# Performance work log

Hardware: AMD Instinct MI355X
Metric: run time of the kernel (lower is better)

Reference implementation:

```python
import jax, jax.numpy as jnp
import numpy as np

B, C, H, W = 4, 128, 256, 256
N, NPOS, KS = 4000, 8, 3
CH = 2 * NPOS  # mask=False -> 2*n_pos offset channels


def setup_inputs() -> dict:
    key = jax.random.key(0)
    ks = jax.random.split(key, 8)
    x = jax.random.normal(ks[0], (B, C, H, W), jnp.float32)
    keypoints = jax.random.uniform(ks[1], (B, N, 2), jnp.float32) * 2.0 - 1.0  # [-1,1]
    w1 = jax.random.normal(ks[2], (CH, C, KS, KS), jnp.float32) * 0.05  # offset conv 3x3
    b1 = jnp.zeros((CH,), jnp.float32)
    w2 = jax.random.normal(ks[3], (CH, CH), jnp.float32) * 0.05        # offset conv 1x1
    b2 = jnp.zeros((CH,), jnp.float32)
    wsf = jax.random.normal(ks[4], (C, C), jnp.float32) * 0.05         # sf_conv 1x1 no bias
    agg_weights = jax.random.uniform(ks[5], (NPOS, C, C), jnp.float32)  # torch.rand init
    return {"x": x, "keypoints": keypoints, "w1": w1, "b1": b1, "w2": w2,
            "b2": b2, "wsf": wsf, "agg_weights": agg_weights}


def _bilinear_sample(img, px, py):
    """grid_sample(mode=bilinear, align_corners=True, padding=zeros) at pixel coords.
    img: (C,H,W); px,py: (M,). Returns (C,M)."""
    c, h, w = img.shape
    x0f = jnp.floor(px); y0f = jnp.floor(py)
    x0 = x0f.astype(jnp.int32); y0 = y0f.astype(jnp.int32)
    wx1 = px - x0f; wx0 = 1.0 - wx1
    wy1 = py - y0f; wy0 = 1.0 - wy1

    def tap(xi, yi, wgt):
        valid = ((xi >= 0) & (xi < w) & (yi >= 0) & (yi < h)).astype(img.dtype)
        v = img[:, jnp.clip(yi, 0, h - 1), jnp.clip(xi, 0, w - 1)]  # (C,M)
        return v * (wgt * valid)

    return (tap(x0, y0, wx0 * wy0) + tap(x0 + 1, y0, wx1 * wy0)
            + tap(x0, y0 + 1, wx0 * wy1) + tap(x0 + 1, y0 + 1, wx1 * wy1))


def _per_image(xi, kpts, w1, b1, w2, b2, wsf, agg_weights):
    wh = jnp.array([W - 1.0, H - 1.0], xi.dtype)
    max_offset = max(H, W) / 4.0
    kwh = (kpts / 2.0 + 0.5) * wh                      # (N,2) pixel coords, >=0
    rc = kwh.astype(jnp.int32)                          # .long() trunc (positive)
    corner = jnp.trunc(rc.astype(jnp.float32) - KS / 2.0 + 1.0).astype(jnp.int32)
    cx = jnp.clip(corner[:, 0], 0, W - 1 - KS)
    cy = jnp.clip(corner[:, 1], 0, H - 1 - KS)
    ar = jnp.arange(KS)
    # patch[n,c,a,b] = xi[c, cy_n+a, cx_n+b]
    patch = xi[:, (cy[:, None] + ar)[:, :, None], (cx[:, None] + ar)[:, None, :]]  # (C,N,KS,KS)
    patch = patch.transpose(1, 0, 2, 3)                 # (N,C,KS,KS)
    # offset network: 3x3 conv (valid) on 3x3 patch == full contraction, then ReLU, 1x1 conv
    h1 = jax.nn.relu(jnp.einsum('nchw,ochw->no', patch, w1) + b1)
    off = jnp.clip(h1 @ w2.T + b2, -max_offset, max_offset)  # (N, 2*NPOS)
    off = off.reshape(-1, 2, NPOS).transpose(0, 2, 1)        # (N,NPOS,2)
    # deform sampling positions; torch normalizes then grid_sample(align_corners=True)
    # maps exactly back to pixel coords, so sample at pixel coords directly
    pos = kwh[:, None, :] + off                              # (N,NPOS,2)
    feats = _bilinear_sample(xi, pos[..., 0].reshape(-1), pos[..., 1].reshape(-1))  # (C,N*NPOS)
    feats = feats.reshape(C, -1, NPOS).transpose(1, 0, 2)    # (N,C,NPOS)
    feats = jax.nn.selu(jnp.einsum('ncp,dc->ndp', feats, wsf))
    descs = jnp.einsum('ncp,pcd->nd', feats, agg_weights)    # (N,C)
    descs = descs / jnp.maximum(jnp.linalg.norm(descs, axis=1, keepdims=True), 1e-12)
    return descs, off


def reference(x, keypoints, w1, b1, w2, b2, wsf, agg_weights):
    f = jax.vmap(lambda xi, k: _per_image(xi, k, w1, b1, w2, b2, wsf, agg_weights))
    descriptors, offsets = f(x, keypoints)
    return descriptors, offsets  # (B,N,C), (B,N,NPOS,2)
```

## Files before the change

kernel.cpp:

```cpp
#include <hip/hip_runtime.h>
#include <math.h>

#define BB 4
#define CC 128
#define HH 256
#define WW 256
#define NN 4000
#define NPOS 8
#define KS 3
#define HWSZ (HH*WW)

#define SELU_ALPHA 1.6732632423543772f
#define SELU_SCALE 1.0507009873554805f
#define MAX_OFFSET 64.0f

typedef unsigned short ushort_t;
typedef short short8 __attribute__((ext_vector_type(8)));
typedef float f32x4 __attribute__((ext_vector_type(4)));
typedef unsigned short ushort4_t __attribute__((ext_vector_type(4)));
typedef unsigned short ushort8_t __attribute__((ext_vector_type(8)));

#define XT_ELEMS    ((size_t)BB*HH*WW*CC)
#define WSFBF_ELEMS ((size_t)CC*CC)
#define AGGT_ELEMS  ((size_t)NPOS*CC*CC)
#define W1T_ELEMS   ((size_t)16*CC*9)
#define WS_NEEDED   ((XT_ELEMS+WSFBF_ELEMS+AGGT_ELEMS+W1T_ELEMS)*sizeof(ushort_t))

__device__ __forceinline__ ushort_t f2bf(float f) {
    unsigned u = __builtin_bit_cast(unsigned, f);
    unsigned r = (u + 0x7FFFu + ((u >> 16) & 1u)) >> 16;
    return (ushort_t)r;
}
__device__ __forceinline__ float bf2f(ushort_t u) {
    return __builtin_bit_cast(float, ((unsigned)u) << 16);
}

__global__ __launch_bounds__(256) void k0p(
    const float* __restrict__ x, ushort_t* __restrict__ xt,
    const float* __restrict__ wsf, const float* __restrict__ agg,
    const float* __restrict__ w1,
    ushort_t* __restrict__ wsf_bf, ushort_t* __restrict__ aggT_bf,
    ushort_t* __restrict__ w1t_bf)
{
    int blk = blockIdx.x;
    const int t = threadIdx.x;
    if (blk >= BB * HH * 4) {
        int i = (blk - BB * HH * 4) * 256 + t;
        if (i < CC * CC) wsf_bf[i] = f2bf(wsf[i]);
        if (i < NPOS * CC * CC) {
            int p = i >> 14, d = (i >> 7) & 127, c = i & 127;
            aggT_bf[i] = f2bf(agg[(p << 14) + (c << 7) + d]);
        }
        if (i < 16 * 1152) {
            int o = i / 1152, e = i - o * 1152, k = e >> 7, c = e & 127;
            w1t_bf[i] = f2bf(w1[o * 1152 + c * 9 + k]);
        }
        return;
    }
    int xc = blk & 3, y = (blk >> 2) & 255, b = blk >> 10;
    int x0 = xc * 64;
    __shared__ ushort_t lds[64][136];

    const float* xb = x + (size_t)b * CC * HWSZ + (size_t)y * WW + x0;
    for (int v = t; v < 2048; v += 256) {
        int c = v >> 4, xo4 = v & 15;
        float4 val = *(const float4*)(xb + (size_t)c * HWSZ + xo4 * 4);
        lds[xo4*4+0][c] = f2bf(val.x);
        lds[xo4*4+1][c] = f2bf(val.y);
        lds[xo4*4+2][c] = f2bf(val.z);
        lds[xo4*4+3][c] = f2bf(val.w);
    }
    __syncthreads();
    ushort_t* outb = xt + ((size_t)b * HWSZ + (size_t)y * WW + x0) * CC;
    for (int v = t; v < 2048; v += 256) {
        int xo = v >> 5, c4 = v & 31;
        ushort4_t val;
        val[0] = lds[xo][c4*4+0];
        val[1] = lds[xo][c4*4+1];
        val[2] = lds[xo][c4*4+2];
        val[3] = lds[xo][c4*4+3];
        *(ushort4_t*)(outb + (size_t)xo * CC + c4 * 4) = val;
    }
}

__global__ __launch_bounds__(256, 2) void k14_fused(
    const ushort_t* __restrict__ xt, const float* __restrict__ kpts,
    const ushort_t* __restrict__ w1t_bf, const float* __restrict__ b1,
    const float* __restrict__ w2, const float* __restrict__ b2,
    const ushort_t* __restrict__ wsf_bf, const ushort_t* __restrict__ aggT_bf,
    float* __restrict__ out_desc, float* __restrict__ out_off)
{
    const int t    = threadIdx.x;
    const int wv   = t >> 6;
    const int lane = t & 63;
    const int m    = lane & 15;
    const int q    = lane >> 4;
    const int n0   = blockIdx.x * 16;
    const int b    = n0 / NN;
    const ushort_t* xb = xt + (size_t)b * HWSZ * CC;

    __shared__ ushort_t fg[CC * CC];
    union PT {
        float partials[4][16][16];
        struct { int tapoff[128][4]; float tapw[128][4]; } tp;
    };
    __shared__ PT    upt;
    __shared__ float h1f[16][17];
    __shared__ float offs[16][16];
    __shared__ float kw[16][2];
    __shared__ int   cxy[16][2];
    __shared__ float wsum[4][16];
    __shared__ float rn[16];

    if (t < 16) {
        float kx = kpts[(size_t)(n0 + t) * 2 + 0];
        float ky = kpts[(size_t)(n0 + t) * 2 + 1];
        float kwx = (kx * 0.5f + 0.5f) * (float)(WW - 1);
        float kwy = (ky * 0.5f + 0.5f) * (float)(HH - 1);
        kw[t][0] = kwx; kw[t][1] = kwy;
        int rcx = (int)kwx, rcy = (int)kwy;
        int cx = (int)truncf((float)rcx - 0.5f);
        int cy = (int)truncf((float)rcy - 0.5f);
        cxy[t][0] = min(max(cx, 0), WW - 1 - KS);
        cxy[t][1] = min(max(cy, 0), HH - 1 - KS);
    }
    __syncthreads();

    {
        int px0 = cxy[m][0], py0 = cxy[m][1];
        const ushort_t* brow = w1t_bf + m * 1152 + wv * 288 + q * 8;
        short8 a0, a1, a2, a3, a4, a5, a6, a7, a8;
        #define LOAD_A(idx, dst) { \
            int e = wv * 288 + (idx) * 32 + q * 8; \
            int k = e >> 7, c = e & 127; \
            int kd = k / 3, kx2 = k - kd * 3; \
            dst = *(const short8*)(xb + ((size_t)((py0 + kd) * WW + px0 + kx2)) * CC + c); }
        LOAD_A(0, a0) LOAD_A(1, a1) LOAD_A(2, a2) LOAD_A(3, a3) LOAD_A(4, a4)
        LOAD_A(5, a5) LOAD_A(6, a6) LOAD_A(7, a7) LOAD_A(8, a8)
        #undef LOAD_A
        f32x4 hacc = {0.f, 0.f, 0.f, 0.f};
        #define MF(idx, areg) { \
            short8 bfr = *(const short8*)(brow + (idx) * 32); \
            hacc = __builtin_amdgcn_mfma_f32_16x16x32_bf16(areg, bfr, hacc, 0, 0, 0); }
        MF(0, a0) MF(1, a1) MF(2, a2) MF(3, a3) MF(4, a4)
        MF(5, a5) MF(6, a6) MF(7, a7) MF(8, a8)
        #undef MF
        #pragma unroll
        for (int r = 0; r < 4; ++r) upt.partials[wv][q * 4 + r][m] = hacc[r];
    }
    __syncthreads();
    {
        int kp = t >> 4, o = t & 15;
        float h = upt.partials[0][kp][o] + upt.partials[1][kp][o]
                + upt.partials[2][kp][o] + upt.partials[3][kp][o] + b1[o];
        h1f[kp][o] = fmaxf(h, 0.f);
    }
    __syncthreads();
    {
        int kp = t >> 4, j = t & 15;
        float s = b2[j];
        #pragma unroll
        for (int o = 0; o < 16; ++o) s += h1f[kp][o] * w2[j * 16 + o];
        s = fminf(fmaxf(s, -MAX_OFFSET), MAX_OFFSET);
        offs[kp][j] = s;
        int p = j & 7, comp = j >> 3;
        out_off[((size_t)(n0 + kp) * 8 + p) * 2 + comp] = s;
    }
    __syncthreads();

    if (t < 128) {
        int kp = t >> 3, p = t & 7;
        float px = kw[kp][0] + offs[kp][p];
        float py = kw[kp][1] + offs[kp][8 + p];
        float x0f = floorf(px), y0f = floorf(py);
        int x0 = (int)x0f, y0 = (int)y0f;
        float wx1 = px - x0f, wx0 = 1.f - wx1;
        float wy1 = py - y0f, wy0 = 1.f - wy1;
        int x0c = min(max(x0, 0), WW - 1);
        int x1c = min(max(x0 + 1, 0), WW - 1);
        int y0c = min(max(y0, 0), HH - 1);
        int y1c = min(max(y0 + 1, 0), HH - 1);
        float vx0 = (x0 >= 0 && x0 < WW) ? 1.f : 0.f;
        float vx1 = (x0 + 1 >= 0 && x0 + 1 < WW) ? 1.f : 0.f;
        float vy0 = (y0 >= 0 && y0 < HH) ? 1.f : 0.f;
        float vy1 = (y0 + 1 >= 0 && y0 + 1 < HH) ? 1.f : 0.f;
        upt.tp.tapoff[t][0] = (y0c * WW + x0c) * CC;
        upt.tp.tapoff[t][1] = (y0c * WW + x1c) * CC;
        upt.tp.tapoff[t][2] = (y1c * WW + x0c) * CC;
        upt.tp.tapoff[t][3] = (y1c * WW + x1c) * CC;
        upt.tp.tapw[t][0] = wx0 * wy0 * vx0 * vy0;
        upt.tp.tapw[t][1] = wx1 * wy0 * vx1 * vy0;
        upt.tp.tapw[t][2] = wx0 * wy1 * vx0 * vy1;
        upt.tp.tapw[t][3] = wx1 * wy1 * vx1 * vy1;
    }
    __syncthreads();

    {
        const int grp = t >> 4;
        const int cl  = t & 15;
        #pragma unroll
        for (int half = 0; half < 2; ++half) {
            ushort8_t tv0[4], tv1[4], tv2[4], tv3[4];
            float4 twv[4];
            #pragma unroll
            for (int i = 0; i < 4; ++i) {
                int pair = (half * 4 + i) * 16 + grp;
                const int* to = upt.tp.tapoff[pair];
                twv[i] = *(const float4*)upt.tp.tapw[pair];
                tv0[i] = *(const ushort8_t*)(xb + to[0] + cl * 8);
                tv1[i] = *(const ushort8_t*)(xb + to[1] + cl * 8);
                tv2[i] = *(const ushort8_t*)(xb + to[2] + cl * 8);
                tv3[i] = *(const ushort8_t*)(xb + to[3] + cl * 8);
            }
            #pragma unroll
            for (int i = 0; i < 4; ++i) {
                int pair = (half * 4 + i) * 16 + grp;
                float w00 = twv[i].x, w01 = twv[i].y, w10 = twv[i].z, w11 = twv[i].w;
                ushort8_t out;
                #pragma unroll
                for (int j = 0; j < 8; ++j) {
                    float v = bf2f(tv0[i][j]) * w00;
                    v += bf2f(tv1[i][j]) * w01;
                    v += bf2f(tv2[i][j]) * w10;
                    v += bf2f(tv3[i][j]) * w11;
                    out[j] = f2bf(v);
                }
                unsigned byte = ((unsigned)(pair * 256 + cl * 16))
                              ^ (((unsigned)(pair & 7)) << 4);
                *(ushort8_t*)((char*)fg + byte) = out;
            }
        }
    }
    __syncthreads();

    for (int rti = 0; rti < 2; ++rti) {
        int rt = wv * 2 + rti;
        int r  = rt * 16 + m;
        unsigned key = ((unsigned)(r & 7)) << 4;
        short8 afr[4];
        #pragma unroll
        for (int kk = 0; kk < 4; ++kk) {
            unsigned byte = ((unsigned)(r * 256 + q * 16 + kk * 64)) ^ key;
            afr[kk] = *(const short8*)((const char*)fg + byte);
        }
        for (int ct = 0; ct < 8; ++ct) {
            const ushort_t* brow = wsf_bf + (ct * 16 + m) * CC + q * 8;
            f32x4 acc = {0.f, 0.f, 0.f, 0.f};
            #pragma unroll
            for (int kk = 0; kk < 4; ++kk) {
                short8 bfr = *(const short8*)(brow + kk * 32);
                acc = __builtin_amdgcn_mfma_f32_16x16x32_bf16(afr[kk], bfr, acc, 0, 0, 0);
            }
            #pragma unroll
            for (int rr = 0; rr < 4; ++rr) {
                float s = acc[rr];
                s = (s > 0.f) ? (SELU_SCALE * s)
                              : (SELU_SCALE * SELU_ALPHA * (expf(s) - 1.f));
                int row = rt * 16 + q * 4 + rr;
                int col = ct * 16 + m;
                unsigned byte = ((unsigned)(row * 256 + col * 2))
                              ^ (((unsigned)((row >> 3) & 7)) << 4);
                *(ushort_t*)((char*)fg + byte) = f2bf(s);
            }
        }
    }
    __syncthreads();

    f32x4 acc2[2];
    acc2[0] = (f32x4){0.f, 0.f, 0.f, 0.f};
    acc2[1] = (f32x4){0.f, 0.f, 0.f, 0.f};
    const int ctbase = wv * 2;
    for (int kk = 0; kk < 32; ++kk) {
        int p    = kk >> 2;
        int rowA = m * 8 + p;
        unsigned byte = ((unsigned)(rowA * 256 + (kk & 3) * 64 + q * 16))
                      ^ (((unsigned)((rowA >> 3) & 7)) << 4);
        short8 afr = *(const short8*)((const char*)fg + byte);
        #pragma unroll
        for (int i = 0; i < 2; ++i) {
            int ct = ctbase + i;
            const ushort_t* brow = aggT_bf + (size_t)(p * CC + ct * 16 + m) * CC
                                 + (kk & 3) * 32 + q * 8;
            short8 bfr = *(const short8*)brow;
            acc2[i] = __builtin_amdgcn_mfma_f32_16x16x32_bf16(afr, bfr, acc2[i], 0, 0, 0);
        }
    }

    {
        float ss[4];
        #pragma unroll
        for (int rr = 0; rr < 4; ++rr)
            ss[rr] = acc2[0][rr] * acc2[0][rr] + acc2[1][rr] * acc2[1][rr];
        #pragma unroll
        for (int mask = 1; mask <= 8; mask <<= 1) {
            #pragma unroll
            for (int rr = 0; rr < 4; ++rr) ss[rr] += __shfl_xor(ss[rr], mask);
        }
        if (m == 0) {
            #pragma unroll
            for (int rr = 0; rr < 4; ++rr) wsum[wv][q * 4 + rr] = ss[rr];
        }
    }
    __syncthreads();
    if (t < 16) {
        float tot = wsum[0][t] + wsum[1][t] + wsum[2][t] + wsum[3][t];
        rn[t] = 1.0f / fmaxf(sqrtf(tot), 1e-12f);
    }
    __syncthreads();
    {
        #pragma unroll
        for (int i = 0; i < 2; ++i) {
            int col = (ctbase + i) * 16 + m;
            #pragma unroll
            for (int rr = 0; rr < 4; ++rr) {
                int n = q * 4 + rr;
                out_desc[(size_t)(n0 + n) * CC + col] = acc2[i][rr] * rn[n];
            }
        }
    }
}

__global__ __launch_bounds__(256, 4) void sddh_baseline(
    const float* __restrict__ x, const float* __restrict__ keypoints,
    const float* __restrict__ w1, const float* __restrict__ b1,
    const float* __restrict__ w2, const float* __restrict__ b2,
    const float* __restrict__ wsf, const float* __restrict__ agg,
    float* __restrict__ out_desc, float* __restrict__ out_off)
{
    const int bn = blockIdx.x;
    const int b  = bn / NN;
    const int t  = threadIdx.x;
    const float* xi = x + (size_t)b * CC * HWSZ;

    __shared__ float patch[CC * 9];
    __shared__ float conv_part[16][17];
    __shared__ float h1s[16];
    __shared__ float offs[16];
    __shared__ float feats[CC][NPOS];
    __shared__ float cpart2[CC][NPOS];
    __shared__ float g[CC][NPOS];
    __shared__ float dpart[CC];
    __shared__ float desc[CC];
    __shared__ float sq[128];
    __shared__ float kxy[2];

    if (t == 0) {
        float kx = keypoints[(size_t)bn * 2 + 0];
        float ky = keypoints[(size_t)bn * 2 + 1];
        kxy[0] = (kx * 0.5f + 0.5f) * (float)(WW - 1);
        kxy[1] = (ky * 0.5f + 0.5f) * (float)(HH - 1);
    }
    __syncthreads();
    const float kwx = kxy[0], kwy = kxy[1];
    const int rcx = (int)kwx, rcy = (int)kwy;
    int cx = (int)truncf((float)rcx - 0.5f);
    int cy = (int)truncf((float)rcy - 0.5f);
    cx = min(max(cx, 0), WW - 1 - KS);
    cy = min(max(cy, 0), HH - 1 - KS);

    for (int e = t; e < CC * 9; e += 256) {
        int c = e / 9, k = e % 9;
        int dy = k / 3, dx = k % 3;
        patch[e] = xi[(size_t)c * HWSZ + (cy + dy) * WW + (cx + dx)];
    }
    __syncthreads();
    {
        int o = t & 15, j = t >> 4;
        float acc = 0.f;
        const float* wo = w1 + o * (CC * 9);
        for (int e = j; e < CC * 9; e += 16) acc += patch[e] * wo[e];
        conv_part[o][j] = acc;
    }
    __syncthreads();
    if (t < 16) {
        float s = b1[t];
        #pragma unroll
        for (int j = 0; j < 16; j++) s += conv_part[t][j];
        h1s[t] = fmaxf(s, 0.f);
    }
    __syncthreads();
    if (t < 16) {
        float s = b2[t];
        #pragma unroll
        for (int k = 0; k < 16; k++) s += h1s[k] * w2[t * 16 + k];
        s = fminf(fmaxf(s, -MAX_OFFSET), MAX_OFFSET);
        offs[t] = s;
        int idx = (t < 8) ? (bn * 16 + t * 2) : (bn * 16 + (t - 8) * 2 + 1);
        out_off[idx] = s;
    }
    __syncthreads();

    for (int e = t; e < CC * NPOS; e += 256) {
        int c = e & 127, p = e >> 7;
        float px = kwx + offs[p];
        float py = kwy + offs[8 + p];
        float x0f = floorf(px), y0f = floorf(py);
        int x0 = (int)x0f, y0 = (int)y0f;
        float wx1 = px - x0f, wx0 = 1.f - wx1;
        float wy1 = py - y0f, wy0 = 1.f - wy1;
        const float* xc = xi + (size_t)c * HWSZ;
        int x0c = min(max(x0, 0), WW - 1);
        int x1c = min(max(x0 + 1, 0), WW - 1);
        int y0c = min(max(y0, 0), HH - 1);
        int y1c = min(max(y0 + 1, 0), HH - 1);
        float vx0 = (x0 >= 0 && x0 < WW) ? 1.f : 0.f;
        float vx1 = (x0 + 1 >= 0 && x0 + 1 < WW) ? 1.f : 0.f;
        float vy0 = (y0 >= 0 && y0 < HH) ? 1.f : 0.f;
        float vy1 = (y0 + 1 >= 0 && y0 + 1 < HH) ? 1.f : 0.f;
        float v = 0.f;
        v += xc[y0c * WW + x0c] * (wx0 * wy0) * (vx0 * vy0);
        v += xc[y0c * WW + x1c] * (wx1 * wy0) * (vx1 * vy0);
        v += xc[y1c * WW + x0c] * (wx0 * wy1) * (vx0 * vy1);
        v += xc[y1c * WW + x1c] * (wx1 * wy1) * (vx1 * vy1);
        feats[c][p] = v;
    }
    __syncthreads();
    {
        int d = t & 127, chalf = t >> 7;
        float acc[NPOS];
        #pragma unroll
        for (int p = 0; p < NPOS; p++) acc[p] = 0.f;
        const float* wrow = wsf + d * CC;
        int c0 = chalf * 64;
        for (int c = c0; c < c0 + 64; c++) {
            float wv = wrow[c];
            #pragma unroll
            for (int p = 0; p < NPOS; p++) acc[p] += feats[c][p] * wv;
        }
        if (chalf) {
            #pragma unroll
            for (int p = 0; p < NPOS; p++) cpart2[d][p] = acc[p];
        }
        __syncthreads();
        if (!chalf) {
            #pragma unroll
            for (int p = 0; p < NPOS; p++) {
                float s = acc[p] + cpart2[d][p];
                s = (s > 0.f) ? (SELU_SCALE * s)
                              : (SELU_SCALE * SELU_ALPHA * (expf(s) - 1.f));
                g[d][p] = s;
            }
        }
    }
    __syncthreads();
    {
        int d = t & 127, half = t >> 7;
        float acc = 0.f;
        int p0 = half * 4;
        for (int p = p0; p < p0 + 4; p++) {
            const float* ap = agg + (size_t)p * CC * CC;
            for (int e = 0; e < CC; e++) acc += g[e][p] * ap[e * CC + d];
        }
        if (half) dpart[d] = acc;
        __syncthreads();
        if (!half) {
            float v = acc + dpart[d];
            desc[d] = v;
            sq[d] = v * v;
        }
    }
    __syncthreads();
    if (t < 64) sq[t] += sq[t + 64]; __syncthreads();
    if (t < 32) sq[t] += sq[t + 32]; __syncthreads();
    if (t < 16) sq[t] += sq[t + 16]; __syncthreads();
    if (t < 8)  sq[t] += sq[t + 8];  __syncthreads();
    if (t < 4)  sq[t] += sq[t + 4];  __syncthreads();
    if (t < 2)  sq[t] += sq[t + 2];  __syncthreads();
    if (t == 0) sq[0] = fmaxf(sqrtf(sq[0] + sq[1]), 1e-12f);
    __syncthreads();
    if (t < 128) out_desc[(size_t)bn * CC + t] = desc[t] / sq[0];
}

extern "C" void kernel_launch(void* const* d_in, const int* in_sizes, int n_in,
                              void* d_out, int out_size, void* d_ws, size_t ws_size,
                              hipStream_t stream) {
    const float* x    = (const float*)d_in[0];
    const float* kpts = (const float*)d_in[1];
    const float* w1   = (const float*)d_in[2];
    const float* b1   = (const float*)d_in[3];
    const float* w2   = (const float*)d_in[4];
    const float* b2   = (const float*)d_in[5];
    const float* wsf  = (const float*)d_in[6];
    const float* agg  = (const float*)d_in[7];

    float* out_desc = (float*)d_out;
    float* out_off  = (float*)d_out + (size_t)BB * NN * CC;

    if (ws_size < WS_NEEDED) {
        hipLaunchKernelGGL(sddh_baseline, dim3(BB * NN), dim3(256), 0, stream,
                           x, kpts, w1, b1, w2, b2, wsf, agg, out_desc, out_off);
        return;
    }

    ushort_t* xt      = (ushort_t*)d_ws;
    ushort_t* wsf_bf  = xt + XT_ELEMS;
    ushort_t* aggT_bf = wsf_bf + WSFBF_ELEMS;
    ushort_t* w1t_bf  = aggT_bf + AGGT_ELEMS;

    hipLaunchKernelGGL(k0p, dim3(BB * HH * 4 + 512), dim3(256), 0, stream,
                       x, xt, wsf, agg, w1, wsf_bf, aggT_bf, w1t_bf);
    hipLaunchKernelGGL(k14_fused, dim3(BB * NN / 16), dim3(256), 0, stream,
                       xt, kpts, w1t_bf, b1, w2, b2, wsf_bf, aggT_bf,
                       out_desc, out_off);
}
```

Baseline: 101.6 us.

## Bucket-sort keypoints by spatial tile and swizzle block order for locality

An extra block in the prep kernel counting-sorts all keypoints into 32x32-pixel spatial buckets per batch and writes a permutation. The fused kernel processes keypoints in permuted order, so each 16-keypoint block gathers from nearby pixels, and it swizzles block IDs across 8 groups. The aim is better L2/cache reuse of the channel-last bf16 feature gathers. The cost is one serial single-block sort inside the prep kernel, which may become the critical path, plus scattered output writes.

```diff
diff --git a/kernel.cpp b/kernel.cpp
--- a/kernel.cpp
+++ b/kernel.cpp
@@ -24,7 +24,9 @@
 #define WSFBF_ELEMS ((size_t)CC*CC)
 #define AGGT_ELEMS  ((size_t)NPOS*CC*CC)
 #define W1T_ELEMS   ((size_t)16*CC*9)
-#define WS_NEEDED   ((XT_ELEMS+WSFBF_ELEMS+AGGT_ELEMS+W1T_ELEMS)*sizeof(ushort_t))
+#define PERM_ELEMS  ((size_t)BB*NN)
+#define WS_NEEDED   ((XT_ELEMS+WSFBF_ELEMS+AGGT_ELEMS+W1T_ELEMS)*sizeof(ushort_t) \
+                     + PERM_ELEMS*sizeof(int))
 
 __device__ __forceinline__ ushort_t f2bf(float f) {
     unsigned u = __builtin_bit_cast(unsigned, f);
@@ -35,15 +37,49 @@
     return __builtin_bit_cast(float, ((unsigned)u) << 16);
 }
 
+__device__ __forceinline__ int kp_bucket(const float* __restrict__ kpts, int i) {
+    float kx = kpts[(size_t)i * 2 + 0];
+    float ky = kpts[(size_t)i * 2 + 1];
+    float kwx = (kx * 0.5f + 0.5f) * (float)(WW - 1);
+    float kwy = (ky * 0.5f + 0.5f) * (float)(HH - 1);
+    int rcx = (int)kwx, rcy = (int)kwy;
+    int b = i / NN;
+    return b * 64 + ((rcy >> 5) << 3) + (rcx >> 5);
+}
+
 __global__ __launch_bounds__(256) void k0p(
     const float* __restrict__ x, ushort_t* __restrict__ xt,
     const float* __restrict__ wsf, const float* __restrict__ agg,
-    const float* __restrict__ w1,
+    const float* __restrict__ w1, const float* __restrict__ kpts,
     ushort_t* __restrict__ wsf_bf, ushort_t* __restrict__ aggT_bf,
-    ushort_t* __restrict__ w1t_bf)
+    ushort_t* __restrict__ w1t_bf, int* __restrict__ perm)
 {
     int blk = blockIdx.x;
     const int t = threadIdx.x;
+
+    if (blk == BB * HH * 4 + 512) {
+        __shared__ int hist[256];
+        __shared__ int base[256];
+        hist[t] = 0;
+        __syncthreads();
+        for (int i = t; i < BB * NN; i += 256)
+            atomicAdd(&hist[kp_bucket(kpts, i)], 1);
+        __syncthreads();
+        if (t == 0) {
+            int acc = 0;
+            #pragma unroll 8
+            for (int i = 0; i < 256; ++i) { base[i] = acc; acc += hist[i]; }
+        }
+        __syncthreads();
+        hist[t] = 0;
+        __syncthreads();
+        for (int i = t; i < BB * NN; i += 256) {
+            int bk = kp_bucket(kpts, i);
+            int pos = base[bk] + atomicAdd(&hist[bk], 1);
+            perm[pos] = i;
+        }
+        return;
+    }
     if (blk >= BB * HH * 4) {
         int i = (blk - BB * HH * 4) * 256 + t;
         if (i < CC * CC) wsf_bf[i] = f2bf(wsf[i]);
@@ -88,6 +124,7 @@
     const ushort_t* __restrict__ w1t_bf, const float* __restrict__ b1,
     const float* __restrict__ w2, const float* __restrict__ b2,
     const ushort_t* __restrict__ wsf_bf, const ushort_t* __restrict__ aggT_bf,
+    const int* __restrict__ perm,
     float* __restrict__ out_desc, float* __restrict__ out_off)
 {
     const int t    = threadIdx.x;
@@ -95,9 +132,9 @@
     const int lane = t & 63;
     const int m    = lane & 15;
     const int q    = lane >> 4;
-    const int n0   = blockIdx.x * 16;
-    const int b    = n0 / NN;
-    const ushort_t* xb = xt + (size_t)b * HWSZ * CC;
+    const int bid  = blockIdx.x;
+    const int sb   = (bid & 7) * ((BB * NN / 16) >> 3) + (bid >> 3);
+    const int n0   = sb * 16;
 
     __shared__ ushort_t fg[CC * CC];
     union PT {
@@ -109,12 +146,15 @@
     __shared__ float offs[16][16];
     __shared__ float kw[16][2];
     __shared__ int   cxy[16][2];
+    __shared__ int   kpi[16];
     __shared__ float wsum[4][16];
     __shared__ float rn[16];
 
     if (t < 16) {
-        float kx = kpts[(size_t)(n0 + t) * 2 + 0];
-        float ky = kpts[(size_t)(n0 + t) * 2 + 1];
+        int kidx = perm[n0 + t];
+        kpi[t] = kidx;
+        float kx = kpts[(size_t)kidx * 2 + 0];
+        float ky = kpts[(size_t)kidx * 2 + 1];
         float kwx = (kx * 0.5f + 0.5f) * (float)(WW - 1);
         float kwy = (ky * 0.5f + 0.5f) * (float)(HH - 1);
         kw[t][0] = kwx; kw[t][1] = kwy;
@@ -125,6 +165,8 @@
         cxy[t][1] = min(max(cy, 0), HH - 1 - KS);
     }
     __syncthreads();
+    const int b = kpi[0] / NN;
+    const ushort_t* xb = xt + (size_t)b * HWSZ * CC;
 
     {
         int px0 = cxy[m][0], py0 = cxy[m][1];
@@ -164,7 +206,7 @@
         s = fminf(fmaxf(s, -MAX_OFFSET), MAX_OFFSET);
         offs[kp][j] = s;
         int p = j & 7, comp = j >> 3;
-        out_off[((size_t)(n0 + kp) * 8 + p) * 2 + comp] = s;
+        out_off[((size_t)kpi[kp] * 8 + p) * 2 + comp] = s;
     }
     __syncthreads();
 
@@ -314,7 +356,7 @@
             #pragma unroll
             for (int rr = 0; rr < 4; ++rr) {
                 int n = q * 4 + rr;
-                out_desc[(size_t)(n0 + n) * CC + col] = acc2[i][rr] * rn[n];
+                out_desc[(size_t)kpi[n] * CC + col] = acc2[i][rr] * rn[n];
             }
         }
     }
@@ -496,10 +538,11 @@
     ushort_t* wsf_bf  = xt + XT_ELEMS;
     ushort_t* aggT_bf = wsf_bf + WSFBF_ELEMS;
     ushort_t* w1t_bf  = aggT_bf + AGGT_ELEMS;
-
-    hipLaunchKernelGGL(k0p, dim3(BB * HH * 4 + 512), dim3(256), 0, stream,
-                       x, xt, wsf, agg, w1, wsf_bf, aggT_bf, w1t_bf);
+    int*      perm    = (int*)(w1t_bf + W1T_ELEMS);
+
+    hipLaunchKernelGGL(k0p, dim3(BB * HH * 4 + 513), dim3(256), 0, stream,
+                       x, xt, wsf, agg, w1, kpts, wsf_bf, aggT_bf, w1t_bf, perm);
     hipLaunchKernelGGL(k14_fused, dim3(BB * NN / 16), dim3(256), 0, stream,
-                       xt, kpts, w1t_bf, b1, w2, b2, wsf_bf, aggT_bf,
+                       xt, kpts, w1t_bf, b1, w2, b2, wsf_bf, aggT_bf, perm,
                        out_desc, out_off);
 }
```

After: 132.5 us. 30.5% more time.
